# Kernel tuning notes

Measured on AMD Instinct MI355X. Metric: run time of the kernel, lower is better.

## Reference

```python
import jax, jax.numpy as jnp
import numpy as np

NUM_HEADS = 8
HEAD_DIM = 16  # hidden_size 128 / 8 heads
SCALE = float(np.sqrt(HEAD_DIM))


def setup_inputs() -> dict:
    key = jax.random.key(0)
    k1, k2, k3, k4 = jax.random.split(key, 4)
    B, N, H = 1, 50000, 128
    E = 800000
    q = jax.random.normal(k1, (B, N, H), dtype=jnp.float32)
    k = jax.random.normal(k2, (B, N, H), dtype=jnp.float32)
    v = jax.random.normal(k3, (B, N, H), dtype=jnp.float32)
    edge_index = jax.random.randint(k4, (2, E), 0, N, dtype=jnp.int64)
    return {"q": q, "k": k, "v": v, "edge_index": edge_index}


def reference(q, k, v, edge_index):
    B, N, H = q.shape
    total = B * N
    qh = q.reshape(total, NUM_HEADS, HEAD_DIM)
    kh = k.reshape(total, NUM_HEADS, HEAD_DIM)
    vh = v.reshape(total, NUM_HEADS, HEAD_DIM)
    src_idx = edge_index[0]
    dst_idx = edge_index[1]
    src = kh[src_idx]          # [E, heads, d]
    dest = qh[dst_idx]         # [E, heads, d]
    # per-edge scaled dot score, clamped then exponentiated
    score = jnp.sum(src * dest / SCALE, axis=-1, keepdims=True)  # [E, heads, 1]
    score = jnp.exp(jnp.clip(score, -5.0, 5.0))
    msg = vh[src_idx] * score  # [E, heads, d]
    wV = jax.ops.segment_sum(msg, dst_idx, num_segments=total)    # [total, heads, d]
    Z = jax.ops.segment_sum(score, dst_idx, num_segments=total)   # [total, heads, 1]
    x = wV / (Z + 1e-6)
    return x.reshape(B, N, NUM_HEADS * HEAD_DIM)
```

## Files before the change

kernel.cpp:

```cpp
#include <hip/hip_runtime.h>

#define HID 128
#define CHUNK 16384
#define CSHIFT 14
#define MAXW 25088
#define WH 12544

typedef unsigned short u16;
typedef unsigned int u32;

__device__ __forceinline__ float lof(u32 w) { return __uint_as_float(w << 16); }
__device__ __forceinline__ float hif(u32 w) { return __uint_as_float(w & 0xFFFF0000u); }
__device__ __forceinline__ u16 f2bf(float f) {
    u32 x = __float_as_uint(f);
    return (u16)((x + 0x7FFF + ((x >> 16) & 1)) >> 16);
}

__global__ __launch_bounds__(1024) void histpack_kernel(
        const int* __restrict__ ei, u32* __restrict__ Hp, u16* __restrict__ lrank,
        const float* __restrict__ kin, const float* __restrict__ vin, u16* __restrict__ kv,
        int E, int W, int N, int histBlocks) {
    __shared__ u32 hcnt[WH];
    if ((int)blockIdx.x < histBlocks) {
        int c = blockIdx.x >> 1;
        int h = blockIdx.x & 1;
        int Wh = (W + 1) >> 1;
        int base = h * Wh;
        int wlen = min(Wh, W - base);
        for (int j = threadIdx.x; j < wlen; j += 1024) hcnt[j] = 0;
        __syncthreads();
        int beg = c << CSHIFT;
        int end = min(E, beg + CHUNK);
        for (int i = beg + (int)threadIdx.x; i < end; i += 1024) {
            int d = ei[E + i];
            int w = d >> 1;
            if (w >= base && w < base + wlen) {
                u32 sh = (u32)(d & 1) << 4;
                u32 old = atomicAdd(&hcnt[w - base], 1u << sh);
                lrank[i] = (u16)((old >> sh) & 0xFFFFu);
            }
        }
        __syncthreads();
        for (int j = threadIdx.x; j < wlen; j += 1024)
            Hp[(size_t)c * W + base + j] = hcnt[j];
    } else {
        int g = ((int)blockIdx.x - histBlocks) * 1024 + (int)threadIdx.x;
        int node = g >> 6, l = g & 63;
        if (node >= N) return;
        float2 kk = ((const float2*)(kin + (long long)node * HID))[l];
        float2 vv = ((const float2*)(vin + (long long)node * HID))[l];
        ushort4 o;
        o.x = f2bf(kk.x * 0.25f);
        o.y = f2bf(kk.y * 0.25f);
        o.z = f2bf(vv.x);
        o.w = f2bf(vv.y);
        ((ushort4*)(kv + (long long)node * 256))[l] = o;
    }
}

__global__ __launch_bounds__(1024) void scan_fused_kernel(u32* __restrict__ Hp,
        int* __restrict__ offsets, int* __restrict__ partials, int W, int NB, int N) {
    __shared__ int sdata[1024];
    int tid = threadIdx.x;
    int j = blockIdx.x * 1024 + tid;
    u32 lo = 0, hi = 0;
    if (j < W) {
        int c = 0;
        for (; c + 8 <= NB; c += 8) {
            u32 w[8];
#pragma unroll
            for (int t = 0; t < 8; t++) w[t] = Hp[(size_t)(c + t) * W + j];
#pragma unroll
            for (int t = 0; t < 8; t++) {
                Hp[(size_t)(c + t) * W + j] = lo | (hi << 16);
                lo += w[t] & 0xFFFFu;
                hi += w[t] >> 16;
            }
        }
        for (; c < NB; c++) {
            size_t idx = (size_t)c * W + j;
            u32 w = Hp[idx];
            Hp[idx] = lo | (hi << 16);
            lo += w & 0xFFFFu;
            hi += w >> 16;
        }
    }
    int s = (int)(lo + hi);
    sdata[tid] = s;
    __syncthreads();
    for (int off = 1; off < 1024; off <<= 1) {
        int x = sdata[tid];
        int y = (tid >= off) ? sdata[tid - off] : 0;
        __syncthreads();
        sdata[tid] = x + y;
        __syncthreads();
    }
    int excl = sdata[tid] - s;
    if (j < W) {
        int n0 = 2 * j, n1 = 2 * j + 1;
        offsets[n0] = excl;
        if (n1 < N) offsets[n1] = excl + (int)lo;
    }
    if (tid == 1023) partials[blockIdx.x] = sdata[1023];
}

__global__ void scanC_kernel(int* __restrict__ offsets, const int* __restrict__ partials,
                             int M, int E, int nbA) {
    __shared__ int sp[256];
    int tid = threadIdx.x;
    if (tid == 0) {
        int run = 0;
        for (int i = 0; i < nbA; i++) { sp[i] = run; run += partials[i]; }
    }
    __syncthreads();
    int idx = blockIdx.x * blockDim.x + tid;
    if (idx < M) offsets[idx] += sp[idx >> 11];
    if (idx == 0) offsets[M] = E;
}

__global__ void scatter_kernel(const int* __restrict__ ei, const u32* __restrict__ Hp,
                               const u16* __restrict__ lrank, const int* __restrict__ offsets,
                               u16* __restrict__ srcs, int E, int W) {
    int e = blockIdx.x * blockDim.x + threadIdx.x;
    if (e >= E) return;
    int c = e >> CSHIFT;
    int d = ei[E + e];
    u32 sh = (u32)(d & 1) << 4;
    u32 b = (Hp[(size_t)c * W + (d >> 1)] >> sh) & 0xFFFFu;
    int pos = offsets[d] + (int)b + (int)lrank[e];
    srcs[pos] = (u16)ei[e];
}

__global__ __launch_bounds__(128) void reduce_packed(
        const float* __restrict__ q, const u16* __restrict__ kv,
        const int* __restrict__ offsets, const u16* __restrict__ srcs,
        float* __restrict__ out, int N) {
    int node = blockIdx.x * 2 + (threadIdx.x >> 6);
    if (node >= N) return;
    int l = threadIdx.x & 63;
    int m = l & 31;
    int half = l >> 5;

    float4 qv = ((const float4*)(q + (long long)node * HID))[m];
    const char* kvb = (const char*)kv;
    u32 laneoff = (u32)m << 4;
    float4 acc = make_float4(0.0f, 0.0f, 0.0f, 0.0f);
    float z = 0.0f;

    int beg = offsets[node];
    int end = offsets[node + 1];
    int i = beg;

#define GLOAD(s_) (*(const uint4*)(kvb + (((u32)(s_) << 9) + laneoff)))

    for (; i + 8 <= end; i += 8) {
        u32 sA0 = srcs[i + 0], sB0 = srcs[i + 1];
        u32 sA1 = srcs[i + 2], sB1 = srcs[i + 3];
        u32 sA2 = srcs[i + 4], sB2 = srcs[i + 5];
        u32 sA3 = srcs[i + 6], sB3 = srcs[i + 7];
        uint4 a0 = GLOAD(half ? sB0 : sA0);
        uint4 a1 = GLOAD(half ? sB1 : sA1);
        uint4 a2 = GLOAD(half ? sB2 : sA2);
        uint4 a3 = GLOAD(half ? sB3 : sA3);

        float p0 = lof(a0.x) * qv.x + hif(a0.x) * qv.y + lof(a0.z) * qv.z + hif(a0.z) * qv.w;
        float p1 = lof(a1.x) * qv.x + hif(a1.x) * qv.y + lof(a1.z) * qv.z + hif(a1.z) * qv.w;
        float p2 = lof(a2.x) * qv.x + hif(a2.x) * qv.y + lof(a2.z) * qv.z + hif(a2.z) * qv.w;
        float p3 = lof(a3.x) * qv.x + hif(a3.x) * qv.y + lof(a3.z) * qv.z + hif(a3.z) * qv.w;

        p0 += __shfl_xor(p0, 1); p1 += __shfl_xor(p1, 1);
        p2 += __shfl_xor(p2, 1); p3 += __shfl_xor(p3, 1);
        p0 += __shfl_xor(p0, 2); p1 += __shfl_xor(p1, 2);
        p2 += __shfl_xor(p2, 2); p3 += __shfl_xor(p3, 2);

        float c0 = __expf(fminf(fmaxf(p0, -5.0f), 5.0f));
        float c1 = __expf(fminf(fmaxf(p1, -5.0f), 5.0f));
        float c2 = __expf(fminf(fmaxf(p2, -5.0f), 5.0f));
        float c3 = __expf(fminf(fmaxf(p3, -5.0f), 5.0f));

        acc.x += lof(a0.y) * c0 + lof(a1.y) * c1 + lof(a2.y) * c2 + lof(a3.y) * c3;
        acc.y += hif(a0.y) * c0 + hif(a1.y) * c1 + hif(a2.y) * c2 + hif(a3.y) * c3;
        acc.z += lof(a0.w) * c0 + lof(a1.w) * c1 + lof(a2.w) * c2 + lof(a3.w) * c3;
        acc.w += hif(a0.w) * c0 + hif(a1.w) * c1 + hif(a2.w) * c2 + hif(a3.w) * c3;
        z += c0 + c1 + c2 + c3;
    }
    for (; i < end; i += 2) {
        int idx = i + half;
        bool ok = idx < end;
        u32 s = srcs[ok ? idx : i];
        uint4 a = GLOAD(s);
        float p = lof(a.x) * qv.x + hif(a.x) * qv.y + lof(a.z) * qv.z + hif(a.z) * qv.w;
        p += __shfl_xor(p, 1);
        p += __shfl_xor(p, 2);
        float c = __expf(fminf(fmaxf(p, -5.0f), 5.0f));
        c = ok ? c : 0.0f;
        acc.x += lof(a.y) * c;
        acc.y += hif(a.y) * c;
        acc.z += lof(a.w) * c;
        acc.w += hif(a.w) * c;
        z += c;
    }
#undef GLOAD

    acc.x += __shfl_xor(acc.x, 32);
    acc.y += __shfl_xor(acc.y, 32);
    acc.z += __shfl_xor(acc.z, 32);
    acc.w += __shfl_xor(acc.w, 32);
    z     += __shfl_xor(z, 32);

    if (half == 0) {
        float inv = 1.0f / (z + 1e-6f);
        ((float4*)(out + (long long)node * HID))[m] =
            make_float4(acc.x * inv, acc.y * inv, acc.z * inv, acc.w * inv);
    }
}


__global__ void count_kernel(const int* __restrict__ ei, int* __restrict__ counts,
                             int* __restrict__ pos, int E) {
    int e = blockIdx.x * blockDim.x + threadIdx.x;
    if (e < E) pos[e] = atomicAdd(&counts[ei[E + e]], 1);
}

__global__ void fill_kernel(const int* __restrict__ ei, const int* __restrict__ offsets,
                            const int* __restrict__ pos, int* __restrict__ srcs, int E) {
    int e = blockIdx.x * blockDim.x + threadIdx.x;
    if (e < E) srcs[offsets[ei[E + e]] + pos[e]] = ei[e];
}

__global__ __launch_bounds__(256) void reduce_f32(
        const float* __restrict__ q, const float* __restrict__ k,
        const float* __restrict__ v, const int* __restrict__ offsets,
        const int* __restrict__ srcs, float* __restrict__ out, int N) {
    int node = blockIdx.x * 4 + (threadIdx.x >> 6);
    if (node >= N) return;
    int l = threadIdx.x & 63;
    float2 qv = ((const float2*)(q + (long long)node * HID))[l];
    float accx = 0.0f, accy = 0.0f, z = 0.0f;
    int beg = offsets[node], end = offsets[node + 1];
    for (int i = beg; i < end; i++) {
        int s = srcs[i];
        float2 kk = ((const float2*)(k + (long long)s * HID))[l];
        float2 vv = ((const float2*)(v + (long long)s * HID))[l];
        float p = (kk.x * qv.x + kk.y * qv.y) * 0.25f;
        p += __shfl_xor(p, 1);
        p += __shfl_xor(p, 2);
        p += __shfl_xor(p, 4);
        float c = __expf(fminf(fmaxf(p, -5.0f), 5.0f));
        accx += vv.x * c; accy += vv.y * c; z += c;
    }
    float inv = 1.0f / (z + 1e-6f);
    ((float2*)(out + (long long)node * HID))[l] = make_float2(accx * inv, accy * inv);
}

__global__ void scanA_kernel(const u32* __restrict__ counts, int* __restrict__ offsets,
                             int* __restrict__ partials, int M) {
    __shared__ int sdata[256];
    int tid = threadIdx.x;
    int base = blockIdx.x * 2048 + tid * 8;
    int v[8];
    int tsum = 0;
    for (int j = 0; j < 8; j++) {
        int idx = base + j;
        v[j] = (idx < M) ? (int)counts[idx] : 0;
        tsum += v[j];
    }
    sdata[tid] = tsum;
    __syncthreads();
    for (int off = 1; off < 256; off <<= 1) {
        int x = sdata[tid];
        int y = (tid >= off) ? sdata[tid - off] : 0;
        __syncthreads();
        sdata[tid] = x + y;
        __syncthreads();
    }
    int excl = sdata[tid] - tsum;
    for (int j = 0; j < 8; j++) {
        int idx = base + j;
        if (idx < M) offsets[idx] = excl;
        excl += v[j];
    }
    if (tid == 255) partials[blockIdx.x] = sdata[255];
}

extern "C" void kernel_launch(void* const* d_in, const int* in_sizes, int n_in,
                              void* d_out, int out_size, void* d_ws, size_t ws_size,
                              hipStream_t stream) {
    const float* q = (const float*)d_in[0];
    const float* k = (const float*)d_in[1];
    const float* v = (const float*)d_in[2];
    const int* ei = (const int*)d_in[3];
    float* out = (float*)d_out;

    int E = in_sizes[3] / 2;
    int N = in_sizes[0] / HID;

    int eblocks = (E + 255) / 256;
    int nbA = (N + 2047) / 2048;
    int nblocksN = (N + 255) / 256;

    int W = (N + 1) / 2;
    int NB = (E + CHUNK - 1) >> CSHIFT;
    int nbF = (W + 1023) / 1024;

    size_t kv_bytes = (size_t)N * 256 * sizeof(u16);
    size_t need = kv_bytes + ((size_t)NB * W + N + 1 + 256) * 4
                + 2 * ((size_t)E + 8) * 2 + 64;

    bool primary = (((W + 1) >> 1) <= WH) && (nbF <= 256) && (ws_size >= need);

    if (primary) {
        u16* kv = (u16*)d_ws;
        u32* Hp = (u32*)((char*)d_ws + kv_bytes);
        int* offsets = (int*)(Hp + (size_t)NB * W);
        int* partials = offsets + N + 1;
        u16* lrank = (u16*)(partials + 256);
        u16* srcs = lrank + ((E + 8) & ~1);

        int histBlocks = NB * 2;
        int packBlocks = (N * 64 + 1023) / 1024;

        histpack_kernel<<<histBlocks + packBlocks, 1024, 0, stream>>>(
            ei, Hp, lrank, k, v, kv, E, W, N, histBlocks);
        scan_fused_kernel<<<nbF, 1024, 0, stream>>>(Hp, offsets, partials, W, NB, N);
        scanC_kernel<<<nblocksN, 256, 0, stream>>>(offsets, partials, N, E, nbF);
        scatter_kernel<<<eblocks, 256, 0, stream>>>(ei, Hp, lrank, offsets, srcs, E, W);
        int rgrid = (N + 1) / 2;
        reduce_packed<<<rgrid, 128, 0, stream>>>(q, kv, offsets, srcs, out, N);
    } else {
        int* counts = (int*)d_ws;
        int* offsets = counts + N;
        int* partials = offsets + N + 1;
        int* pos = partials + 256;
        int* srcs = pos + E;

        hipMemsetAsync(counts, 0, (size_t)N * sizeof(int), stream);
        count_kernel<<<eblocks, 256, 0, stream>>>(ei, counts, pos, E);
        scanA_kernel<<<nbA, 256, 0, stream>>>((const u32*)counts, offsets, partials, N);
        scanC_kernel<<<nblocksN, 256, 0, stream>>>(offsets, partials, N, E, nbA);
        fill_kernel<<<eblocks, 256, 0, stream>>>(ei, offsets, pos, srcs, E);
        int rgrid = (N + 3) / 4;
        reduce_f32<<<rgrid, 256, 0, stream>>>(q, k, v, offsets, srcs, out, N);
    }
}
```

Measured before the change: 104.8 us.

## Drop scanC pass by folding block partial prefix into scatter and reduce; quarter histogram windows

```diff
diff --git a/kernel.cpp b/kernel.cpp
--- a/kernel.cpp
+++ b/kernel.cpp
@@ -3,8 +3,7 @@
 #define HID 128
 #define CHUNK 16384
 #define CSHIFT 14
-#define MAXW 25088
-#define WH 12544
+#define WH 6272
 
 typedef unsigned short u16;
 typedef unsigned int u32;
@@ -14,6 +13,17 @@
 __device__ __forceinline__ u16 f2bf(float f) {
     u32 x = __float_as_uint(f);
     return (u16)((x + 0x7FFF + ((x >> 16) & 1)) >> 16);
+}
+
+__device__ __forceinline__ int block_base(const int* __restrict__ partials,
+                                          int nbF, int lane, int b) {
+    int pv = (lane < nbF) ? partials[lane] : 0;
+    for (int off = 1; off < 64; off <<= 1) {
+        int y = __shfl_up(pv, off);
+        if (lane >= off) pv += y;
+    }
+    int bb = __shfl(pv, b > 0 ? b - 1 : 0);
+    return b > 0 ? bb : 0;
 }
 
 __global__ __launch_bounds__(1024) void histpack_kernel(
@@ -22,11 +32,11 @@
         int E, int W, int N, int histBlocks) {
     __shared__ u32 hcnt[WH];
     if ((int)blockIdx.x < histBlocks) {
-        int c = blockIdx.x >> 1;
-        int h = blockIdx.x & 1;
-        int Wh = (W + 1) >> 1;
-        int base = h * Wh;
-        int wlen = min(Wh, W - base);
+        int c = blockIdx.x >> 2;
+        int h = blockIdx.x & 3;
+        int Wq = (W + 3) >> 2;
+        int base = h * Wq;
+        int wlen = min(Wq, W - base);
         for (int j = threadIdx.x; j < wlen; j += 1024) hcnt[j] = 0;
         __syncthreads();
         int beg = c << CSHIFT;
@@ -104,51 +114,61 @@
     if (tid == 1023) partials[blockIdx.x] = sdata[1023];
 }
 
-__global__ void scanC_kernel(int* __restrict__ offsets, const int* __restrict__ partials,
-                             int M, int E, int nbA) {
-    __shared__ int sp[256];
-    int tid = threadIdx.x;
-    if (tid == 0) {
-        int run = 0;
-        for (int i = 0; i < nbA; i++) { sp[i] = run; run += partials[i]; }
-    }
-    __syncthreads();
-    int idx = blockIdx.x * blockDim.x + tid;
-    if (idx < M) offsets[idx] += sp[idx >> 11];
-    if (idx == 0) offsets[M] = E;
-}
-
 __global__ void scatter_kernel(const int* __restrict__ ei, const u32* __restrict__ Hp,
                                const u16* __restrict__ lrank, const int* __restrict__ offsets,
-                               u16* __restrict__ srcs, int E, int W) {
+                               const int* __restrict__ partials, u16* __restrict__ srcs,
+                               int E, int W, int nbF) {
+    int lane = threadIdx.x & 63;
+    int pv = (lane < nbF) ? partials[lane] : 0;
+    for (int off = 1; off < 64; off <<= 1) {
+        int y = __shfl_up(pv, off);
+        if (lane >= off) pv += y;
+    }
     int e = blockIdx.x * blockDim.x + threadIdx.x;
     if (e >= E) return;
     int c = e >> CSHIFT;
     int d = ei[E + e];
+    int blk = d >> 11;
+    int bb = __shfl(pv, blk > 0 ? blk - 1 : 0);
+    int basev = blk > 0 ? bb : 0;
     u32 sh = (u32)(d & 1) << 4;
     u32 b = (Hp[(size_t)c * W + (d >> 1)] >> sh) & 0xFFFFu;
-    int pos = offsets[d] + (int)b + (int)lrank[e];
+    int pos = offsets[d] + basev + (int)b + (int)lrank[e];
     srcs[pos] = (u16)ei[e];
 }
 
 __global__ __launch_bounds__(128) void reduce_packed(
         const float* __restrict__ q, const u16* __restrict__ kv,
-        const int* __restrict__ offsets, const u16* __restrict__ srcs,
-        float* __restrict__ out, int N) {
+        const int* __restrict__ offsets, const int* __restrict__ partials,
+        const u16* __restrict__ srcs, float* __restrict__ out, int N, int E, int nbF) {
     int node = blockIdx.x * 2 + (threadIdx.x >> 6);
     if (node >= N) return;
     int l = threadIdx.x & 63;
     int m = l & 31;
     int half = l >> 5;
 
+    int pv = (l < nbF) ? partials[l] : 0;
+    for (int off = 1; off < 64; off <<= 1) {
+        int y = __shfl_up(pv, off);
+        if (l >= off) pv += y;
+    }
+    int b0 = node >> 11;
+    int bb0 = __shfl(pv, b0 > 0 ? b0 - 1 : 0);
+    int beg = offsets[node] + (b0 > 0 ? bb0 : 0);
+    int end;
+    int m1 = node + 1;
+    if (m1 == N) end = E;
+    else {
+        int b1 = m1 >> 11;
+        int bb1 = __shfl(pv, b1 > 0 ? b1 - 1 : 0);
+        end = offsets[m1] + (b1 > 0 ? bb1 : 0);
+    }
+
     float4 qv = ((const float4*)(q + (long long)node * HID))[m];
     const char* kvb = (const char*)kv;
     u32 laneoff = (u32)m << 4;
     float4 acc = make_float4(0.0f, 0.0f, 0.0f, 0.0f);
     float z = 0.0f;
-
-    int beg = offsets[node];
-    int end = offsets[node + 1];
     int i = beg;
 
 #define GLOAD(s_) (*(const uint4*)(kvb + (((u32)(s_) << 9) + laneoff)))
@@ -283,6 +303,20 @@
     if (tid == 255) partials[blockIdx.x] = sdata[255];
 }
 
+__global__ void scanC_kernel(int* __restrict__ offsets, const int* __restrict__ partials,
+                             int M, int E, int nbA) {
+    __shared__ int sp[256];
+    int tid = threadIdx.x;
+    if (tid == 0) {
+        int run = 0;
+        for (int i = 0; i < nbA; i++) { sp[i] = run; run += partials[i]; }
+    }
+    __syncthreads();
+    int idx = blockIdx.x * blockDim.x + tid;
+    if (idx < M) offsets[idx] += sp[idx >> 11];
+    if (idx == 0) offsets[M] = E;
+}
+
 extern "C" void kernel_launch(void* const* d_in, const int* in_sizes, int n_in,
                               void* d_out, int out_size, void* d_ws, size_t ws_size,
                               hipStream_t stream) {
@@ -307,7 +341,7 @@
     size_t need = kv_bytes + ((size_t)NB * W + N + 1 + 256) * 4
                 + 2 * ((size_t)E + 8) * 2 + 64;
 
-    bool primary = (((W + 1) >> 1) <= WH) && (nbF <= 256) && (ws_size >= need);
+    bool primary = (((W + 3) >> 2) <= WH) && (nbF <= 64) && (ws_size >= need);
 
     if (primary) {
         u16* kv = (u16*)d_ws;
@@ -317,16 +351,17 @@
         u16* lrank = (u16*)(partials + 256);
         u16* srcs = lrank + ((E + 8) & ~1);
 
-        int histBlocks = NB * 2;
+        int histBlocks = NB * 4;
         int packBlocks = (N * 64 + 1023) / 1024;
 
         histpack_kernel<<<histBlocks + packBlocks, 1024, 0, stream>>>(
             ei, Hp, lrank, k, v, kv, E, W, N, histBlocks);
         scan_fused_kernel<<<nbF, 1024, 0, stream>>>(Hp, offsets, partials, W, NB, N);
-        scanC_kernel<<<nblocksN, 256, 0, stream>>>(offsets, partials, N, E, nbF);
-        scatter_kernel<<<eblocks, 256, 0, stream>>>(ei, Hp, lrank, offsets, srcs, E, W);
+        scatter_kernel<<<eblocks, 256, 0, stream>>>(ei, Hp, lrank, offsets, partials,
+                                                    srcs, E, W, nbF);
         int rgrid = (N + 1) / 2;
-        reduce_packed<<<rgrid, 128, 0, stream>>>(q, kv, offsets, srcs, out, N);
+        reduce_packed<<<rgrid, 128, 0, stream>>>(q, kv, offsets, partials, srcs,
+                                                 out, N, E, nbF);
     } else {
         int* counts = (int*)d_ws;
         int* offsets = counts + N;
```

New measurement: 105.4 us. No clear change (+0.5%).
